# Optimization experiments

Measured on AMD Instinct MI355X. Metric: run time of the kernel, lower is better.

Reference implementation:

```python
import jax, jax.numpy as jnp
import numpy as np

S_LEN = 1024; HIDDEN = 2048; VOCAB = 32000; DFF = 6144
NK = 8; NV = 16; DK = 128; DV = 128; CONV_K = 4
CONV_DIM = 2 * NK * DK + NV * DV  # 4096
NQ = 16; NKV = 2; HD = 128; MAX_KV = 4096; SP = 512; CHUNK = 64


def silu(x):
    return x * jax.nn.sigmoid(x)


def rmsnorm(x, w, eps=1e-6):
    xf = x.astype(jnp.float32)
    return (xf * jax.lax.rsqrt(jnp.mean(xf * xf, -1, keepdims=True) + eps)) * w


def gated_rmsnorm(x, z, w, eps=1e-6):
    xf = x.astype(jnp.float32) * silu(z.astype(jnp.float32))
    return (xf * jax.lax.rsqrt(jnp.mean(xf * xf, -1, keepdims=True) + eps)) * w


def rotate_half(x):
    a, b = jnp.split(x, 2, -1)
    return jnp.concatenate([-b, a], -1)


def chunk_gated_delta_rule(q, k, v, g, beta, init_state, chunk=CHUNK):
    # q,k: [B,S,H,Dk]; v: [B,S,H,Dv]; g,beta: [B,S,H]; init_state: [B,H,Dk,Dv]
    q = q / jnp.sqrt(jnp.sum(q * q, -1, keepdims=True) + 1e-6)  # qk l2norm
    k = k / jnp.sqrt(jnp.sum(k * k, -1, keepdims=True) + 1e-6)
    tr = lambda x: x.transpose(0, 2, 1, 3).astype(jnp.float32)
    q, k, v = tr(q), tr(k), tr(v)
    g = g.transpose(0, 2, 1).astype(jnp.float32)
    beta = beta.transpose(0, 2, 1).astype(jnp.float32)
    B, H, S, Dk = q.shape
    Dv = v.shape[-1]
    N = S // chunk  # S is a multiple of chunk here (no padding needed)
    q = q * Dk ** -0.5
    rc = lambda x: x.reshape(B, H, N, chunk, x.shape[-1])
    q, k, v = rc(q), rc(k), rc(v)
    g = jnp.cumsum(g.reshape(B, H, N, chunk), -1)  # cumulative log-decay within chunk
    beta = beta.reshape(B, H, N, chunk)
    kb = k * beta[..., None]
    vb = v * beta[..., None]
    ii = jnp.arange(chunk)
    lower = ii[:, None] >= ii[None, :]
    strict = ii[:, None] > ii[None, :]
    decay = jnp.where(lower, jnp.exp(g[..., :, None] - g[..., None, :]), 0.0)
    # strictly-lower A; T = (I - A)^{-1} (exact triangular solve == converged Neumann series)
    A = -jnp.where(strict, jnp.einsum('bhnik,bhnjk->bhnij', kb, k) * decay, 0.0)
    eye = jnp.eye(chunk, dtype=jnp.float32)
    T = jax.scipy.linalg.solve_triangular(eye - A, jnp.broadcast_to(eye, A.shape), lower=True)
    w = jnp.einsum('bhnij,bhnjd->bhnid', T, vb)
    kc = jnp.einsum('bhnij,bhnjd->bhnid', T, kb * jnp.exp(g)[..., None])
    mv = lambda x: jnp.moveaxis(x, 2, 0)

    def step(state, xs):
        qi, ki, wi, kci, gi, di = xs
        attn = jnp.where(lower, jnp.einsum('bhik,bhjk->bhij', qi, ki) * di, 0.0)
        v_new = wi - jnp.einsum('bhik,bhkd->bhid', kci, state)
        out = jnp.einsum('bhik,bhkd->bhid', qi * jnp.exp(gi)[..., None], state) \
            + jnp.einsum('bhij,bhjd->bhid', attn, v_new)
        gl = gi[..., -1]
        kd = ki * jnp.exp(gl[..., None] - gi)[..., None]
        state = state * jnp.exp(gl)[..., None, None] + jnp.einsum('bhik,bhid->bhkd', kd, v_new)
        return state, out

    final, outs = jax.lax.scan(step, init_state.astype(jnp.float32),
                               (mv(q), mv(k), mv(w), mv(kc), mv(g), mv(decay)))
    out = jnp.moveaxis(outs, 0, 2).reshape(B, H, S, Dv).transpose(0, 2, 1, 3)  # [B,S,H,Dv]
    return out, final


def mlp(x, gw, uw, dw):
    return (silu(x @ gw) * (x @ uw)) @ dw


def model_forward(input_ids, start_pos, rope_cos, rope_sin, attn_mask, conv_state, rec_state,
                  key_cache, value_cache, embed_w, dl_ln_w, dl_qkv_w, conv_w, conv_b, dl_z_w,
                  dl_b_w, dl_a_w, A_log, dt_bias, dn_norm_w, dl_out_w, dl_post_ln_w, dl_gate_w,
                  dl_up_w, dl_down_w, al_ln_w, q_w, q_norm_w, k_w, k_norm_w, v_w, o_w,
                  al_post_ln_w, al_gate_w, al_up_w, al_down_w, final_norm_w, lm_head_w):
    B, S = input_ids.shape
    hidden = embed_w[input_ids]
    # ---------------- DeltaNet (linear attention) layer ----------------
    res = hidden
    x = rmsnorm(hidden, dl_ln_w)
    mixed = (x @ dl_qkv_w).transpose(0, 2, 1)             # [B, CONV_DIM, S]
    padded = jnp.concatenate([conv_state, mixed], -1)      # [B, CONV_DIM, K+S]
    L = padded.shape[-1] - (CONV_K - 1)
    conv = conv_b[:, None] + sum(conv_w[:, kk][:, None] * padded[:, :, kk:kk + L]
                                 for kk in range(CONV_K))  # depthwise conv1d
    mixed = silu(conv[:, :, -S:]).transpose(0, 2, 1)
    new_conv = padded[:, :, -CONV_K:]
    kd = NK * DK
    qq = mixed[..., :kd].reshape(B, S, NK, DK)
    kk_ = mixed[..., kd:2 * kd].reshape(B, S, NK, DK)
    vv = mixed[..., 2 * kd:].reshape(B, S, NV, DV)
    z = (x @ dl_z_w).reshape(B, S, NV, DV)
    beta = jax.nn.sigmoid(x @ dl_b_w)
    a = (x @ dl_a_w).astype(jnp.float32)
    g = -jnp.exp(A_log.astype(jnp.float32)) * jax.nn.softplus(a + dt_bias)
    rep = NV // NK
    qq = jnp.repeat(qq, rep, axis=2)
    kk_ = jnp.repeat(kk_, rep, axis=2)
    core, new_rec = chunk_gated_delta_rule(qq, kk_, vv, g, beta, rec_state)
    core = gated_rmsnorm(core.reshape(-1, DV), z.reshape(-1, DV), dn_norm_w).reshape(B, S, NV * DV)
    hidden = res + core @ dl_out_w
    hidden = hidden + mlp(rmsnorm(hidden, dl_post_ln_w), dl_gate_w, dl_up_w, dl_down_w)
    # ---------------- Full attention layer (gated GQA, KV-cache scatter) ----------------
    res = hidden
    x = rmsnorm(hidden, al_ln_w)
    qg = (x @ q_w).reshape(B, S, NQ, 2 * HD)
    query, gate = jnp.split(qg, 2, -1)
    gate = gate.reshape(B, S, NQ * HD)
    query = rmsnorm(query, q_norm_w).transpose(0, 2, 1, 3)               # [B,NQ,S,HD]
    key_new = rmsnorm((x @ k_w).reshape(B, S, NKV, HD), k_norm_w).transpose(0, 2, 1, 3)
    value_new = (x @ v_w).reshape(B, S, NKV, HD).transpose(0, 2, 1, 3)
    c = rope_cos[:, None]
    sn = rope_sin[:, None]
    query = query * c + rotate_half(query) * sn
    key_new = key_new * c + rotate_half(key_new) * sn
    new_kc = jax.lax.dynamic_update_slice(key_cache, key_new, (0, 0, start_pos, 0))
    new_vc = jax.lax.dynamic_update_slice(value_cache, value_new, (0, 0, start_pos, 0))
    ng = NQ // NKV
    k_rep = jnp.repeat(new_kc, ng, axis=1)
    v_rep = jnp.repeat(new_vc, ng, axis=1)
    scores = jnp.einsum('bhsd,bhtd->bhst', query, k_rep) * HD ** -0.5 + attn_mask
    probs = jax.nn.softmax(scores.astype(jnp.float32), -1).astype(query.dtype)
    ao = jnp.einsum('bhst,bhtd->bhsd', probs, v_rep).transpose(0, 2, 1, 3).reshape(B, S, NQ * HD)
    ao = ao * jax.nn.sigmoid(gate)
    hidden = res + ao @ o_w
    hidden = hidden + mlp(rmsnorm(hidden, al_post_ln_w), al_gate_w, al_up_w, al_down_w)
    logits = rmsnorm(hidden, final_norm_w) @ lm_head_w
    return logits, new_conv, new_rec, new_kc, new_vc


def setup_inputs():
    key = jax.random.key(0)
    ks = iter(jax.random.split(key, 64))
    def rn(shape, s=0.02):
        return jax.random.normal(next(ks), shape, jnp.float32) * s
    input_ids = jax.random.randint(next(ks), (1, S_LEN), 0, VOCAB)
    inv = 1.0 / (10000.0 ** (jnp.arange(0, HD, 2, dtype=jnp.float32) / HD))
    pos = jnp.arange(SP, SP + S_LEN, dtype=jnp.float32)
    fr = pos[:, None] * inv[None, :]
    emb = jnp.concatenate([fr, fr], -1)
    rope_cos = jnp.cos(emb)[None]
    rope_sin = jnp.sin(emb)[None]
    qpos = SP + jnp.arange(S_LEN)
    kpos = jnp.arange(MAX_KV)
    attn_mask = jnp.where(kpos[None, :] <= qpos[:, None], 0.0, -1e9).astype(jnp.float32)[None, None]
    return dict(
        input_ids=input_ids, seq_len=S_LEN, start_pos=SP,
        rope_cos=rope_cos, rope_sin=rope_sin, attn_mask=attn_mask,
        conv_state=rn((1, CONV_DIM, CONV_K), 1.0), rec_state=rn((1, NV, DK, DV), 1.0),
        key_cache=rn((1, NKV, MAX_KV, HD), 1.0), value_cache=rn((1, NKV, MAX_KV, HD), 1.0),
        embed_w=rn((VOCAB, HIDDEN)), dl_ln_w=jnp.ones(HIDDEN),
        dl_qkv_w=rn((HIDDEN, CONV_DIM)), conv_w=rn((CONV_DIM, CONV_K), 0.3),
        conv_b=rn((CONV_DIM,)), dl_z_w=rn((HIDDEN, NV * DV)),
        dl_b_w=rn((HIDDEN, NV)), dl_a_w=rn((HIDDEN, NV)),
        A_log=jnp.log(jnp.linspace(1.0, 8.0, NV)), dt_bias=rn((NV,), 0.1),
        dn_norm_w=jnp.ones(DV), dl_out_w=rn((NV * DV, HIDDEN)),
        dl_post_ln_w=jnp.ones(HIDDEN), dl_gate_w=rn((HIDDEN, DFF)),
        dl_up_w=rn((HIDDEN, DFF)), dl_down_w=rn((DFF, HIDDEN)),
        al_ln_w=jnp.ones(HIDDEN), q_w=rn((HIDDEN, NQ * HD * 2)), q_norm_w=jnp.ones(HD),
        k_w=rn((HIDDEN, NKV * HD)), k_norm_w=jnp.ones(HD), v_w=rn((HIDDEN, NKV * HD)),
        o_w=rn((NQ * HD, HIDDEN)), al_post_ln_w=jnp.ones(HIDDEN),
        al_gate_w=rn((HIDDEN, DFF)), al_up_w=rn((HIDDEN, DFF)), al_down_w=rn((DFF, HIDDEN)),
        final_norm_w=jnp.ones(HIDDEN), lm_head_w=rn((HIDDEN, VOCAB)))


def reference(input_ids, seq_len, start_pos, rope_cos, rope_sin, attn_mask, conv_state,
              rec_state, key_cache, value_cache, embed_w, dl_ln_w, dl_qkv_w, conv_w, conv_b,
              dl_z_w, dl_b_w, dl_a_w, A_log, dt_bias, dn_norm_w, dl_out_w, dl_post_ln_w,
              dl_gate_w, dl_up_w, dl_down_w, al_ln_w, q_w, q_norm_w, k_w, k_norm_w, v_w, o_w,
              al_post_ln_w, al_gate_w, al_up_w, al_down_w, final_norm_w, lm_head_w):
    del seq_len  # unused in original forward body (padding bookkeeping only)
    return model_forward(input_ids, start_pos, rope_cos, rope_sin, attn_mask, conv_state,
                         rec_state, key_cache, value_cache, embed_w, dl_ln_w, dl_qkv_w, conv_w,
                         conv_b, dl_z_w, dl_b_w, dl_a_w, A_log, dt_bias, dn_norm_w, dl_out_w,
                         dl_post_ln_w, dl_gate_w, dl_up_w, dl_down_w, al_ln_w, q_w, q_norm_w,
                         k_w, k_norm_w, v_w, o_w, al_post_ln_w, al_gate_w, al_up_w, al_down_w,
                         final_norm_w, lm_head_w)
```

## Files before the change

### kernel.cpp

```cpp
#include <hip/hip_runtime.h>
#include <math.h>

#define S_LEN 1024
#define HIDN  2048
#define NVH   16
#define CDIM  4096
#define MAXKV 4096
#define SP    512

typedef __attribute__((ext_vector_type(4))) float f32x4v;
typedef _Float16 f16x8 __attribute__((ext_vector_type(8)));
typedef unsigned short ushort_t;

__device__ __forceinline__ unsigned int pack2h(float a, float b) {
  auto h = __builtin_amdgcn_cvt_pkrtz(a, b);
  return __builtin_bit_cast(unsigned int, h);
}
__device__ __forceinline__ ushort_t h16(float x) {
  auto v = __builtin_amdgcn_cvt_pkrtz(x, x);
  return (ushort_t)__builtin_bit_cast(unsigned int, v);
}

template<bool ACC>
__global__ __launch_bounds__(256) void gemm_f16(const float* __restrict__ A,
    const float* __restrict__ B, float* __restrict__ C, int M, int N, int K) {
  __shared__ unsigned int Al[4][128][4];
  __shared__ unsigned int Bl[4][128][4];
  const int tid = threadIdx.x;
  const int gm = M >> 7;
  const int nwg = gridDim.x;
  const int q = nwg >> 3, r = nwg & 7;
  const int xcd = blockIdx.x & 7, ii = blockIdx.x >> 3;
  const int lin = (xcd < r) ? (xcd * (q + 1) + ii)
                            : (r * (q + 1) + (xcd - r) * q + ii);
  const int m0 = (lin % gm) * 128;
  const int n0 = (lin / gm) * 128;
  const int wave = tid >> 6, lane = tid & 63;
  const int wm = (wave >> 1) * 64, wn = (wave & 1) * 64;
  const int lr = lane & 15, lg = lane >> 4;
  const int am = tid >> 1, akb = (tid & 1) * 2;
  const int bn = tid & 127, bkb = (tid >> 7) * 2;
  const float* Ap = A + (size_t)(m0 + am) * K + akb * 8;
  const float* Bp = B + (size_t)(bkb * 8) * N + n0 + bn;
  float ar[16];
  float br[16];
  f32x4v acc[4][4];
  #pragma unroll
  for (int i = 0; i < 4; ++i)
    #pragma unroll
    for (int j = 0; j < 4; ++j)
      #pragma unroll
      for (int r2 = 0; r2 < 4; ++r2) acc[i][j][r2] = 0.f;
  const int NT = K >> 5;
  #pragma unroll
  for (int q2 = 0; q2 < 4; ++q2) *(float4*)&ar[q2 * 4] = *(const float4*)(Ap + q2 * 4);
  #pragma unroll
  for (int j = 0; j < 16; ++j) br[j] = Bp[(size_t)j * N];
  for (int t = 0; t < NT; ++t) {
    __syncthreads();
    *(uint4*)&Al[akb][am][0] = make_uint4(
        pack2h(ar[0], ar[1]), pack2h(ar[2], ar[3]),
        pack2h(ar[4], ar[5]), pack2h(ar[6], ar[7]));
    *(uint4*)&Al[akb + 1][am][0] = make_uint4(
        pack2h(ar[8], ar[9]), pack2h(ar[10], ar[11]),
        pack2h(ar[12], ar[13]), pack2h(ar[14], ar[15]));
    *(uint4*)&Bl[bkb][bn][0] = make_uint4(
        pack2h(br[0], br[1]), pack2h(br[2], br[3]),
        pack2h(br[4], br[5]), pack2h(br[6], br[7]));
    *(uint4*)&Bl[bkb + 1][bn][0] = make_uint4(
        pack2h(br[8], br[9]), pack2h(br[10], br[11]),
        pack2h(br[12], br[13]), pack2h(br[14], br[15]));
    if (t + 1 < NT) {
      Ap += 32; Bp += (size_t)32 * N;
      #pragma unroll
      for (int q2 = 0; q2 < 4; ++q2) *(float4*)&ar[q2 * 4] = *(const float4*)(Ap + q2 * 4);
      #pragma unroll
      for (int j = 0; j < 16; ++j) br[j] = Bp[(size_t)j * N];
    }
    __syncthreads();
    f16x8 af[4], bfr[4];
    #pragma unroll
    for (int mi = 0; mi < 4; ++mi)
      af[mi] = *(const f16x8*)&Al[lg][wm + mi * 16 + lr][0];
    #pragma unroll
    for (int ni = 0; ni < 4; ++ni)
      bfr[ni] = *(const f16x8*)&Bl[lg][wn + ni * 16 + lr][0];
    #pragma unroll
    for (int mi = 0; mi < 4; ++mi)
      #pragma unroll
      for (int ni = 0; ni < 4; ++ni)
        acc[mi][ni] = __builtin_amdgcn_mfma_f32_16x16x32_f16(
            af[mi], bfr[ni], acc[mi][ni], 0, 0, 0);
  }
  #pragma unroll
  for (int mi = 0; mi < 4; ++mi) {
    #pragma unroll
    for (int ni = 0; ni < 4; ++ni) {
      const int rr = m0 + wm + mi * 16 + lg * 4;
      const int cc = n0 + wn + ni * 16 + lr;
      #pragma unroll
      for (int r2 = 0; r2 < 4; ++r2) {
        float* cp = C + (size_t)(rr + r2) * N + cc;
        if (ACC) *cp += acc[mi][ni][r2];
        else     *cp = acc[mi][ni][r2];
      }
    }
  }
}

__global__ __launch_bounds__(256) void embed_k(const int* __restrict__ ids,
    const float* __restrict__ emb, float* __restrict__ hid) {
  int t = blockIdx.x * 256 + threadIdx.x;
  int s = t >> 9;
  int c4 = (t & 511) * 4;
  *(float4*)(hid + (size_t)s * HIDN + c4) =
      *(const float4*)(emb + (size_t)ids[s] * HIDN + c4);
}

__global__ __launch_bounds__(256) void rmsnorm_k(const float* __restrict__ in,
    const float* __restrict__ w, float* __restrict__ out) {
  const int row = blockIdx.x;
  const float* ip = in + (size_t)row * HIDN;
  float ss = 0.f;
  for (int c = threadIdx.x * 4; c < HIDN; c += 1024) {
    float4 v = *(const float4*)(ip + c);
    ss += v.x * v.x + v.y * v.y + v.z * v.z + v.w * v.w;
  }
  #pragma unroll
  for (int o = 32; o > 0; o >>= 1) ss += __shfl_down(ss, o, 64);
  __shared__ float sred[4];
  if ((threadIdx.x & 63) == 0) sred[threadIdx.x >> 6] = ss;
  __syncthreads();
  float tot = sred[0] + sred[1] + sred[2] + sred[3];
  float sc = 1.f / sqrtf(tot * (1.f / HIDN) + 1e-6f);
  for (int c = threadIdx.x * 4; c < HIDN; c += 1024) {
    float4 v = *(const float4*)(ip + c);
    float4 o = make_float4(v.x * sc * w[c], v.y * sc * w[c + 1],
                           v.z * sc * w[c + 2], v.w * sc * w[c + 3]);
    *(float4*)(out + (size_t)row * HIDN + c) = o;
  }
}

__global__ __launch_bounds__(256) void newconv_k(const float* __restrict__ mixed,
                                                 float* __restrict__ nc) {
  int t = blockIdx.x * 256 + threadIdx.x;
  int c = t >> 2, kk = t & 3;
  nc[t] = mixed[(size_t)(1020 + kk) * CDIM + c];
}

__global__ __launch_bounds__(256) void conv_k(const float* __restrict__ mixed,
    const float* __restrict__ cstate, const float* __restrict__ cw,
    const float* __restrict__ cb, float* __restrict__ convo) {
  int idx = blockIdx.x * 256 + threadIdx.x;
  int c = idx & (CDIM - 1);
  int s = idx >> 12;
  float acc = cb[c];
  #pragma unroll
  for (int kk = 0; kk < 4; ++kk) {
    int j = s + 1 + kk;
    float pv = (j < 4) ? cstate[c * 4 + j] : mixed[(size_t)(j - 4) * CDIM + c];
    acc = fmaf(cw[c * 4 + kk], pv, acc);
  }
  convo[(size_t)s * CDIM + c] = acc / (1.f + expf(-acc));
}

__global__ __launch_bounds__(128) void qknorm_k(const float* __restrict__ convo,
    float* __restrict__ qn, float* __restrict__ kn) {
  const int b = blockIdx.x;
  const int h8 = b & 7, s = b >> 3;
  const int d = threadIdx.x;
  float qv = convo[(size_t)s * CDIM + h8 * 128 + d];
  float kv = convo[(size_t)s * CDIM + 1024 + h8 * 128 + d];
  __shared__ float sred[4];
  float pq = qv * qv, pk = kv * kv;
  #pragma unroll
  for (int o = 32; o > 0; o >>= 1) { pq += __shfl_down(pq, o, 64); pk += __shfl_down(pk, o, 64); }
  if ((d & 63) == 0) { sred[d >> 6] = pq; sred[2 + (d >> 6)] = pk; }
  __syncthreads();
// ... 20 lines not shown
    acca = fmaf(xv, aw[(size_t)k * 16 + h], acca);
  }
  rb[part][h] = accb; ra[part][h] = acca;
  __syncthreads();
  if (threadIdx.x < 16) {
    const int hh = threadIdx.x;
    float sb = 0.f, sa = 0.f;
    for (int p = 0; p < 16; ++p) { sb += rb[p][hh]; sa += ra[p][hh]; }
    beta[(size_t)s * 16 + hh] = 1.f / (1.f + expf(-sb));
    float aa = sa + dt_bias[hh];
    float sp = (aa > 20.f) ? aa : log1pf(expf(aa));
    g[(size_t)s * 16 + hh] = -expf(A_log[hh]) * sp;
  }
}

__global__ __launch_bounds__(256) void delta_phase1(
    const float* __restrict__ qn, const float* __restrict__ kn,
    const float* __restrict__ convo, const float* __restrict__ beta,
    const float* __restrict__ g,
    float* __restrict__ Wb, ushort_t* __restrict__ KC16,
    ushort_t* __restrict__ Q16, ushort_t* __restrict__ K16,
    ushort_t* __restrict__ ATT16, float* __restrict__ GCb) {
  __shared__ float sK[64][129];
  __shared__ float sV[64][129];
  __shared__ float sQ[64][129];
  __shared__ float sT[64][64];
  __shared__ float sgc[64], sbeta[64], seg[64], sEgl[64];
  const int blk = blockIdx.x;
  const int n = blk & 15, h = blk >> 4;
  const int hq = h >> 1;
  const int r0 = n * 64;
  const int tid = threadIdx.x;
  const size_t hn = (size_t)h * 16 + n;
  for (int t = tid; t < 2048; t += 256) {
    int i = t >> 5, c4 = (t & 31) * 4;
    float4 kv = *(const float4*)(kn + ((size_t)hq * S_LEN + r0 + i) * 128 + c4);
    float4 qv = *(const float4*)(qn + ((size_t)hq * S_LEN + r0 + i) * 128 + c4);
    float4 vv = *(const float4*)(convo + (size_t)(r0 + i) * CDIM + 2048 + h * 128 + c4);
    sK[i][c4+0]=kv.x; sK[i][c4+1]=kv.y; sK[i][c4+2]=kv.z; sK[i][c4+3]=kv.w;
    sQ[i][c4+0]=qv.x; sQ[i][c4+1]=qv.y; sQ[i][c4+2]=qv.z; sQ[i][c4+3]=qv.w;
    sV[i][c4+0]=vv.x; sV[i][c4+1]=vv.y; sV[i][c4+2]=vv.z; sV[i][c4+3]=vv.w;
  }
  if (tid < 64) sbeta[tid] = beta[(size_t)(r0 + tid) * NVH + h];
  __syncthreads();
  if (tid == 0) {
    float acc = 0.f;
    for (int i = 0; i < 64; ++i) { acc += g[(size_t)(r0 + i) * NVH + h]; sgc[i] = acc; }
  }
  __syncthreads();
  if (tid < 64) {
    seg[tid] = expf(sgc[tid]);
    sEgl[tid] = expf(sgc[63] - sgc[tid]);
  }
  {
    const int ty = tid >> 4, tx = tid & 15;
    float a[4][4] = {};
    #pragma unroll 4
    for (int k = 0; k < 128; ++k) {
      float kr[4], kc_[4];
      #pragma unroll
      for (int di = 0; di < 4; ++di) kr[di] = sK[ty * 4 + di][k];
      #pragma unroll
      for (int dj = 0; dj < 4; ++dj) kc_[dj] = sK[tx * 4 + dj][k];
      #pragma unroll
      for (int di = 0; di < 4; ++di)
        #pragma unroll
        for (int dj = 0; dj < 4; ++dj)
          a[di][dj] = fmaf(kr[di], kc_[dj], a[di][dj]);
    }
    #pragma unroll
    for (int di = 0; di < 4; ++di) {
      int i = ty * 4 + di;
      #pragma unroll
      for (int dj = 0; dj < 4; ++dj) {
        int j = tx * 4 + dj;
        float v;
        if (i > j) v = sbeta[i] * a[di][dj] * expf(sgc[i] - sgc[j]);
        else v = (i == j) ? 1.f : 0.f;
        sT[i][j] = v;
      }
    }
  }
  __syncthreads();
  for (int i = 1; i < 64; ++i) {
    float acc = 0.f;
    const int c = tid;
    const bool act = (c < 64 && c <= i);
    if (act) {
      acc = (c == i) ? 1.f : 0.f;
      for (int j = c; j < i; ++j) acc -= sT[i][j] * sT[j][c];
    }
    __syncthreads();
    if (act) sT[i][c] = acc;
    __syncthreads();
  }
  for (int t = tid; t < 1024; t += 256) {
    int i = t >> 4, dg = (t & 15) * 8;
    float aw[8] = {}, ak[8] = {};
    for (int j = 0; j <= i; ++j) {
      float tv = sT[i][j] * sbeta[j];
      float te = tv * seg[j];
      #pragma unroll
      for (int u = 0; u < 8; ++u) {
        aw[u] = fmaf(tv, sV[j][dg + u], aw[u]);
        ak[u] = fmaf(te, sK[j][dg + u], ak[u]);
      }
    }
    float* wp = Wb + (hn * 64 + i) * 128 + dg;
    *(float4*)wp = make_float4(aw[0], aw[1], aw[2], aw[3]);
    *(float4*)(wp + 4) = make_float4(aw[4], aw[5], aw[6], aw[7]);
    uint4 kc = make_uint4(pack2h(-ak[0], -ak[1]), pack2h(-ak[2], -ak[3]),
                          pack2h(-ak[4], -ak[5]), pack2h(-ak[6], -ak[7]));
    *(uint4*)(KC16 + hn * 8192 + (dg >> 3) * 512 + i * 8) = kc;
  }
  for (int t = tid; t < 1024; t += 256) {
    int i = t >> 4, dg = (t & 15) * 8;
    float e = seg[i];
    uint4 qv = make_uint4(
        pack2h(sQ[i][dg] * e, sQ[i][dg + 1] * e),
        pack2h(sQ[i][dg + 2] * e, sQ[i][dg + 3] * e),
        pack2h(sQ[i][dg + 4] * e, sQ[i][dg + 5] * e),
        pack2h(sQ[i][dg + 6] * e, sQ[i][dg + 7] * e));
    *(uint4*)(Q16 + hn * 8192 + (dg >> 3) * 512 + i * 8) = qv;
  }
  for (int t = tid; t < 1024; t += 256) {
    int kv = t & 127, ib = t >> 7;
    int i0 = ib * 8;
    uint4 kk2 = make_uint4(
        pack2h(sK[i0 + 0][kv] * sEgl[i0 + 0], sK[i0 + 1][kv] * sEgl[i0 + 1]),
        pack2h(sK[i0 + 2][kv] * sEgl[i0 + 2], sK[i0 + 3][kv] * sEgl[i0 + 3]),
        pack2h(sK[i0 + 4][kv] * sEgl[i0 + 4], sK[i0 + 5][kv] * sEgl[i0 + 5]),
        pack2h(sK[i0 + 6][kv] * sEgl[i0 + 6], sK[i0 + 7][kv] * sEgl[i0 + 7]));
    *(uint4*)(K16 + hn * 8192 + ib * 1024 + kv * 8) = kk2;
  }
  __syncthreads();
  {
    const int ty = tid >> 4, tx = tid & 15;
    float a[4][4] = {};
    #pragma unroll 4
    for (int k = 0; k < 128; ++k) {
      float qr[4], kc_[4];
      #pragma unroll
      for (int di = 0; di < 4; ++di) qr[di] = sQ[ty * 4 + di][k];
      #pragma unroll
      for (int dj = 0; dj < 4; ++dj) kc_[dj] = sK[tx * 4 + dj][k];
      #pragma unroll
      for (int di = 0; di < 4; ++di)
        #pragma unroll
        for (int dj = 0; dj < 4; ++dj)
          a[di][dj] = fmaf(qr[di], kc_[dj], a[di][dj]);
    }
    #pragma unroll
    for (int di = 0; di < 4; ++di) {
      int i = ty * 4 + di;
      #pragma unroll
      for (int dj = 0; dj < 4; ++dj) {
        int j = tx * 4 + dj;
        float v = 0.f;
        if (i >= j) v = a[di][dj] * expf(sgc[i] - sgc[j]);
        sT[i][j] = v;
      }
    }
  }
  __syncthreads();
  for (int t = tid; t < 512; t += 256) {
    int i = t >> 3, jb = t & 7;
    const float* ap = &sT[i][jb * 8];
    uint4 av = make_uint4(pack2h(ap[0], ap[1]), pack2h(ap[2], ap[3]),
                          pack2h(ap[4], ap[5]), pack2h(ap[6], ap[7]));
    *(uint4*)(ATT16 + hn * 4096 + jb * 512 + i * 8) = av;
  }
  if (tid < 64) GCb[hn * 64 + tid] = sgc[tid];
}

__global__ __launch_bounds__(256) void delta_phase2(
    const ushort_t* __restrict__ KC16, const ushort_t* __restrict__ Q16,
    const ushort_t* __restrict__ K16, const ushort_t* __restrict__ ATT16,
    const float* __restrict__ Wb, const float* __restrict__ GCb,
// ... 92 lines not shown
        sVn[(row >> 3) * 256 + col * 8 + (row & 7)] = h16(aV[tn][r]);
      }
    __syncthreads();
    f32x4v aO[2];
    #pragma unroll
    for (int tn = 0; tn < 2; ++tn)
      #pragma unroll
      for (int r = 0; r < 4; ++r) aO[tn][r] = 0.f;
    #pragma unroll
    for (int c = 0; c < 4; ++c) {
      f16x8 a = *(const f16x8*)&sQ6[((c * 4 + lg) * 64 + w * 16 + lr) * 8];
      #pragma unroll
      for (int tn = 0; tn < 2; ++tn) {
        f16x8 b = *(const f16x8*)&sS[((c * 4 + lg) * 32 + tn * 16 + lr) * 8];
        aO[tn] = __builtin_amdgcn_mfma_f32_16x16x32_f16(a, b, aO[tn], 0, 0, 0);
      }
    }
    #pragma unroll
    for (int c = 0; c < 2; ++c) {
      f16x8 a = *(const f16x8*)&sAT[((c * 4 + lg) * 64 + w * 16 + lr) * 8];
      #pragma unroll
      for (int tn = 0; tn < 2; ++tn) {
        f16x8 b = *(const f16x8*)&sVn[((c * 4 + lg) * 32 + tn * 16 + lr) * 8];
        aO[tn] = __builtin_amdgcn_mfma_f32_16x16x32_f16(a, b, aO[tn], 0, 0, 0);
      }
    }
    #pragma unroll
    for (int tn = 0; tn < 2; ++tn)
      #pragma unroll
      for (int r = 0; r < 4; ++r) {
        int row = w * 16 + lg * 4 + r;
        core[(size_t)(n * 64 + row) * HIDN + h * 128 + d0 + tn * 16 + lr] = aO[tn][r];
      }
    #pragma unroll
    for (int tm = 0; tm < 2; ++tm)
      #pragma unroll
      for (int tn = 0; tn < 2; ++tn)
        #pragma unroll
        for (int r = 0; r < 4; ++r) aS[tm][tn][r] *= egl;
    #pragma unroll
    for (int tm = 0; tm < 2; ++tm) {
      #pragma unroll
      for (int c = 0; c < 2; ++c) {
        f16x8 a = *(const f16x8*)&sK6[((c * 4 + lg) * 128 + rowS0 + tm * 16 + lr) * 8];
        #pragma unroll
        for (int tn = 0; tn < 2; ++tn) {
          f16x8 b = *(const f16x8*)&sVn[((c * 4 + lg) * 32 + tn * 16 + lr) * 8];
          aS[tm][tn] = __builtin_amdgcn_mfma_f32_16x16x32_f16(a, b, aS[tm][tn], 0, 0, 0);
        }
      }
    }
    __syncthreads();
  }
  #pragma unroll
  for (int tm = 0; tm < 2; ++tm)
    #pragma unroll
    for (int tn = 0; tn < 2; ++tn)
      #pragma unroll
      for (int r = 0; r < 4; ++r) {
        int row = rowS0 + tm * 16 + lg * 4 + r;
        int col = tn * 16 + lr;
        new_rec[((size_t)h * 128 + row) * 128 + d0 + col] = aS[tm][tn][r];
      }
}

__global__ __launch_bounds__(128) void gatedrms_k(float* __restrict__ core,
    const float* __restrict__ z, const float* __restrict__ w) {
  const int b = blockIdx.x;
  const int h = b & 15, s = b >> 4;
  const int d = threadIdx.x;
  size_t idx = (size_t)s * HIDN + h * 128 + d;
  float cv = core[idx], zv = z[idx];
  float xf = cv * (zv / (1.f + expf(-zv)));
  __shared__ float sred[2];
  float ps = xf * xf;
  #pragma unroll
  for (int o = 32; o > 0; o >>= 1) ps += __shfl_down(ps, o, 64);
  if ((d & 63) == 0) sred[d >> 6] = ps;
  __syncthreads();
  float ss = sred[0] + sred[1];
  core[idx] = xf * (1.f / sqrtf(ss * (1.f / 128.f) + 1e-6f)) * w[d];
}

__global__ __launch_bounds__(256) void silumul_k(float* __restrict__ gbuf,
                                                 const float* __restrict__ ubuf) {
  int t = blockIdx.x * 256 + threadIdx.x;
  float4 gv = ((const float4*)gbuf)[t];
  float4 uv = ((const float4*)ubuf)[t];
  gv.x = gv.x / (1.f + expf(-gv.x)) * uv.x;
  gv.y = gv.y / (1.f + expf(-gv.y)) * uv.y;
  gv.z = gv.z / (1.f + expf(-gv.z)) * uv.z;
  gv.w = gv.w / (1.f + expf(-gv.w)) * uv.w;
  ((float4*)gbuf)[t] = gv;
}

__global__ __launch_bounds__(128) void qrope_k(const float* __restrict__ qg,
    const float* __restrict__ qnw, const float* __restrict__ cosb,
    const float* __restrict__ sinb, float* __restrict__ qhat,
    float* __restrict__ agate) {
  const int b = blockIdx.x;
  const int h = b & 15, s = b >> 4;
  const int d = threadIdx.x;
  float qv = qg[(size_t)s * 4096 + h * 256 + d];
  float gv = qg[(size_t)s * 4096 + h * 256 + 128 + d];
  __shared__ float sred[2];
  float ps = qv * qv;
  #pragma unroll
  for (int o = 32; o > 0; o >>= 1) ps += __shfl_down(ps, o, 64);
  if ((d & 63) == 0) sred[d >> 6] = ps;
  __syncthreads();
  float ss = sred[0] + sred[1];
  float qn_ = qv * (1.f / sqrtf(ss * (1.f / 128.f) + 1e-6f)) * qnw[d];
  __shared__ float tmp[128];
  tmp[d] = qn_;
  __syncthreads();
  float other = tmp[d ^ 64];
  float rh = (d < 64) ? -other : other;
  float c = cosb[(size_t)s * 128 + d];
  float sn = sinb[(size_t)s * 128 + d];
  qhat[((size_t)h * S_LEN + s) * 128 + d] = qn_ * c + rh * sn;
  agate[(size_t)s * HIDN + h * 128 + d] = gv;
}

__global__ __launch_bounds__(128) void kvrope_k(const float* __restrict__ kraw,
    const float* __restrict__ vraw, const float* __restrict__ knw,
    const float* __restrict__ cosb, const float* __restrict__ sinb,
    float* __restrict__ kcache, float* __restrict__ vcache) {
  const int b = blockIdx.x;
  const int h2 = b & 1, s = b >> 1;
  const int d = threadIdx.x;
  float kv = kraw[(size_t)s * 256 + h2 * 128 + d];
  __shared__ float sred[2];
  float ps = kv * kv;
  #pragma unroll
  for (int o = 32; o > 0; o >>= 1) ps += __shfl_down(ps, o, 64);
  if ((d & 63) == 0) sred[d >> 6] = ps;
  __syncthreads();
  float ss = sred[0] + sred[1];
  float kn_ = kv * (1.f / sqrtf(ss * (1.f / 128.f) + 1e-6f)) * knw[d];
  __shared__ float tmp[128];
  tmp[d] = kn_;
  __syncthreads();
  float other = tmp[d ^ 64];
  float rh = (d < 64) ? -other : other;
  size_t row = (size_t)h2 * MAXKV + SP + s;
  kcache[row * 128 + d] = kn_ * cosb[(size_t)s * 128 + d] + rh * sinb[(size_t)s * 128 + d];
  vcache[row * 128 + d] = vraw[(size_t)s * 256 + h2 * 128 + d];
}

__global__ __launch_bounds__(256) void attn_k(const float* __restrict__ qhat,
    const float* __restrict__ kcache, const float* __restrict__ vcache,
    const float* __restrict__ agate, float* __restrict__ ao) {
  __shared__ unsigned int Ql[16][64][4];
  __shared__ unsigned int Kl[16][64][4];
  __shared__ unsigned int Vl[8][128][4];
  __shared__ unsigned int Pl[8][64][4];
  const int h = blockIdx.x >> 4, qb = blockIdx.x & 15;
  const int hkv = h >> 3;
  const int tid = threadIdx.x;
  const int wave = tid >> 6, lane = tid & 63;
  const int lr = lane & 15, lg = lane >> 4;
  const float SCALE = 0.08838834764831845f;
  const float* Qb = qhat + ((size_t)h * S_LEN + qb * 64) * 128;
  #pragma unroll
  for (int it = 0; it < 4; ++it) {
    int tt = tid + it * 256;
    int row = tt >> 4, kb = tt & 15;
    float4 a = *(const float4*)(Qb + row * 128 + kb * 8);
    float4 b = *(const float4*)(Qb + row * 128 + kb * 8 + 4);
    *(uint4*)&Ql[kb][row][0] = make_uint4(
        pack2h(a.x * SCALE, a.y * SCALE), pack2h(a.z * SCALE, a.w * SCALE),
        pack2h(b.x * SCALE, b.y * SCALE), pack2h(b.z * SCALE, b.w * SCALE));
  }
  float m_run[4], l_run[4];
  #pragma unroll
  for (int r = 0; r < 4; ++r) { m_run[r] = -3.0e38f; l_run[r] = 0.f; }
  f32x4v accO[8];
  #pragma unroll
// ... 37 lines not shown
    for (int ni = 0; ni < 4; ++ni)
      #pragma unroll
      for (int r = 0; r < 4; ++r) accS[ni][r] = 0.f;
    #pragma unroll
    for (int c = 0; c < 4; ++c) {
      f16x8 aq = *(const f16x8*)&Ql[c * 4 + lg][wave * 16 + lr][0];
      #pragma unroll
      for (int ni = 0; ni < 4; ++ni) {
        f16x8 bk = *(const f16x8*)&Kl[c * 4 + lg][ni * 16 + lr][0];
        accS[ni] = __builtin_amdgcn_mfma_f32_16x16x32_f16(aq, bk, accS[ni], 0, 0, 0);
      }
    }
    const bool boundary = (kt == ntiles - 1);
    float alpha[4];
    #pragma unroll
    for (int r = 0; r < 4; ++r) {
      const int qrow = wave * 16 + lg * 4 + r;
      float tm = -3.0e38f;
      #pragma unroll
      for (int ni = 0; ni < 4; ++ni) {
        if (boundary && (ni * 16 + lr) > qrow) accS[ni][r] = -3.0e38f;
        tm = fmaxf(tm, accS[ni][r]);
      }
      tm = fmaxf(tm, __shfl_xor(tm, 1, 64));
      tm = fmaxf(tm, __shfl_xor(tm, 2, 64));
      tm = fmaxf(tm, __shfl_xor(tm, 4, 64));
      tm = fmaxf(tm, __shfl_xor(tm, 8, 64));
      float mnew = fmaxf(m_run[r], tm);
      alpha[r] = expf(m_run[r] - mnew);
      m_run[r] = mnew;
      float ls = 0.f;
      #pragma unroll
      for (int ni = 0; ni < 4; ++ni) {
        float p = expf(accS[ni][r] - mnew);
        accS[ni][r] = p;
        ls += p;
      }
      ls += __shfl_xor(ls, 1, 64);
      ls += __shfl_xor(ls, 2, 64);
      ls += __shfl_xor(ls, 4, 64);
      ls += __shfl_xor(ls, 8, 64);
      l_run[r] = l_run[r] * alpha[r] + ls;
    }
    {
      _Float16* pp = (_Float16*)Pl;
      #pragma unroll
      for (int ni = 0; ni < 4; ++ni) {
        int key = ni * 16 + lr;
        int base = (key >> 3) * 512 + (key & 7);
        #pragma unroll
        for (int r = 0; r < 4; ++r) {
          int q = wave * 16 + lg * 4 + r;
          pp[base + q * 8] = (_Float16)accS[ni][r];
        }
      }
    }
    #pragma unroll
    for (int nd = 0; nd < 8; ++nd)
      #pragma unroll
      for (int r = 0; r < 4; ++r) accO[nd][r] *= alpha[r];
    #pragma unroll
    for (int c2 = 0; c2 < 2; ++c2) {
      f16x8 ap = *(const f16x8*)&Pl[c2 * 4 + lg][wave * 16 + lr][0];
      #pragma unroll
      for (int nd = 0; nd < 8; ++nd) {
        f16x8 bv = *(const f16x8*)&Vl[c2 * 4 + lg][nd * 16 + lr][0];
        accO[nd] = __builtin_amdgcn_mfma_f32_16x16x32_f16(ap, bv, accO[nd], 0, 0, 0);
      }
    }
  }
  #pragma unroll
  for (int r = 0; r < 4; ++r) {
    const int s = qb * 64 + wave * 16 + lg * 4 + r;
    const float inv = 1.f / l_run[r];
    #pragma unroll
    for (int nd = 0; nd < 8; ++nd) {
      int d = nd * 16 + lr;
      float gv = agate[(size_t)s * HIDN + h * 128 + d];
      ao[(size_t)s * HIDN + h * 128 + d] = accO[nd][r] * inv * (1.f / (1.f + expf(-gv)));
    }
  }
}

static inline void gemm(const float* A, const float* B, float* C,
                        int M, int N, int K, bool acc, hipStream_t st) {
  dim3 g((N / 128) * (M / 128));
  if (acc) hipLaunchKernelGGL((gemm_f16<true>),  g, dim3(256), 0, st, A, B, C, M, N, K);
  else     hipLaunchKernelGGL((gemm_f16<false>), g, dim3(256), 0, st, A, B, C, M, N, K);
}

extern "C" void kernel_launch(void* const* d_in, const int* in_sizes, int n_in,
                              void* d_out, int out_size, void* d_ws, size_t ws_size,
                              hipStream_t stream) {
  (void)in_sizes; (void)n_in; (void)out_size; (void)ws_size;
  const int*   ids         = (const int*)  d_in[0];
  const float* rope_cos    = (const float*)d_in[3];
  const float* rope_sin    = (const float*)d_in[4];
  const float* conv_state  = (const float*)d_in[6];
  const float* rec_state   = (const float*)d_in[7];
  const float* key_cache   = (const float*)d_in[8];
  const float* value_cache = (const float*)d_in[9];
  const float* embed_w     = (const float*)d_in[10];
  const float* dl_ln_w     = (const float*)d_in[11];
  const float* dl_qkv_w    = (const float*)d_in[12];
  const float* conv_w      = (const float*)d_in[13];
  const float* conv_b      = (const float*)d_in[14];
  const float* dl_z_w      = (const float*)d_in[15];
  const float* dl_b_w      = (const float*)d_in[16];
  const float* dl_a_w      = (const float*)d_in[17];
  const float* A_log       = (const float*)d_in[18];
  const float* dt_bias     = (const float*)d_in[19];
  const float* dn_norm_w   = (const float*)d_in[20];
  const float* dl_out_w    = (const float*)d_in[21];
  const float* dl_post_ln  = (const float*)d_in[22];
  const float* dl_gate_w   = (const float*)d_in[23];
  const float* dl_up_w     = (const float*)d_in[24];
  const float* dl_down_w   = (const float*)d_in[25];
  const float* al_ln_w     = (const float*)d_in[26];
  const float* q_w         = (const float*)d_in[27];
  const float* q_norm_w    = (const float*)d_in[28];
  const float* k_w         = (const float*)d_in[29];
  const float* k_norm_w    = (const float*)d_in[30];
  const float* v_w         = (const float*)d_in[31];
  const float* o_w         = (const float*)d_in[32];
  const float* al_post_ln  = (const float*)d_in[33];
  const float* al_gate_w   = (const float*)d_in[34];
  const float* al_up_w     = (const float*)d_in[35];
  const float* al_down_w   = (const float*)d_in[36];
  const float* final_norm  = (const float*)d_in[37];
  const float* lm_head_w   = (const float*)d_in[38];

  float* out = (float*)d_out;
  float* logits   = out;
  float* new_conv = out + 32768000;
  float* new_rec  = out + 32784384;
  float* new_kc   = out + 33046528;
  float* new_vc   = out + 34095104;

  float* A_mixed = logits;
  float* A_convo = logits + 4194304;
  float* A_z     = logits + 8388608;
  float* A_qn    = logits + 10485760;
  float* A_kn    = logits + 11534336;
  float* A_w     = logits + 12582912;
  float* A_kc    = logits + 14680064;
  float* A_att   = logits + 16777216;
  float* A_gc    = logits + 17825792;
  float* A_core  = logits + 17842176;
  float* A_big0  = logits + 19939328;
  float* A_big1  = logits + 26230784;
  float* A_qhat  = A_big1;
  float* A_gate  = A_big1 + 2097152;
  float* A_ao    = A_big1 + 4194304;
  float* A_kraw  = A_mixed;
  float* A_vraw  = A_mixed + 262144;

  ushort_t* KC16  = (ushort_t*)A_kc;
  ushort_t* K16   = (ushort_t*)A_kc + 2097152;
  ushort_t* Q16   = (ushort_t*)A_att;
  ushort_t* ATT16 = (ushort_t*)A_big0;

  float* ws     = (float*)d_ws;
  float* W_hid  = ws;
  float* W_x    = ws + 2097152;
  float* W_beta = ws + 4194304;
  float* W_g    = ws + 4210688;

  hipLaunchKernelGGL(embed_k, dim3(2048), dim3(256), 0, stream, ids, embed_w, W_hid);
  hipLaunchKernelGGL(rmsnorm_k, dim3(1024), dim3(256), 0, stream, W_hid, dl_ln_w, W_x);
  gemm(W_x, dl_qkv_w, A_mixed, 1024, 4096, 2048, false, stream);
  hipLaunchKernelGGL(newconv_k, dim3(64), dim3(256), 0, stream, A_mixed, new_conv);
  hipLaunchKernelGGL(conv_k, dim3(16384), dim3(256), 0, stream,
                     A_mixed, conv_state, conv_w, conv_b, A_convo);
  gemm(W_x, dl_z_w, A_z, 1024, 2048, 2048, false, stream);
  hipLaunchKernelGGL(betag_k, dim3(1024), dim3(256), 0, stream,
                     W_x, dl_b_w, dl_a_w, A_log, dt_bias, W_beta, W_g);
  hipLaunchKernelGGL(qknorm_k, dim3(8192), dim3(128), 0, stream, A_convo, A_qn, A_kn);
  hipLaunchKernelGGL(delta_phase1, dim3(256), dim3(256), 0, stream,
                     A_qn, A_kn, A_convo, W_beta, W_g,
                     A_w, KC16, Q16, K16, ATT16, A_gc);
  hipLaunchKernelGGL(delta_phase2, dim3(64), dim3(256), 0, stream,
                     KC16, Q16, K16, ATT16, A_w, A_gc, rec_state, A_core, new_rec);
  hipLaunchKernelGGL(gatedrms_k, dim3(16384), dim3(128), 0, stream, A_core, A_z, dn_norm_w);
  gemm(A_core, dl_out_w, W_hid, 1024, 2048, 2048, true, stream);
  hipLaunchKernelGGL(rmsnorm_k, dim3(1024), dim3(256), 0, stream, W_hid, dl_post_ln, W_x);
  gemm(W_x, dl_gate_w, A_big0, 1024, 6144, 2048, false, stream);
  gemm(W_x, dl_up_w,   A_big1, 1024, 6144, 2048, false, stream);
  hipLaunchKernelGGL(silumul_k, dim3(6144), dim3(256), 0, stream, A_big0, A_big1);
  gemm(A_big0, dl_down_w, W_hid, 1024, 2048, 6144, true, stream);
  hipLaunchKernelGGL(rmsnorm_k, dim3(1024), dim3(256), 0, stream, W_hid, al_ln_w, W_x);
  gemm(W_x, q_w, A_big0, 1024, 4096, 2048, false, stream);
  hipLaunchKernelGGL(qrope_k, dim3(16384), dim3(128), 0, stream,
                     A_big0, q_norm_w, rope_cos, rope_sin, A_qhat, A_gate);
  gemm(W_x, k_w, A_kraw, 1024, 256, 2048, false, stream);
  gemm(W_x, v_w, A_vraw, 1024, 256, 2048, false, stream);
  hipMemcpyAsync(new_kc, key_cache,   (size_t)2 * MAXKV * 128 * 4, hipMemcpyDeviceToDevice, stream);
  hipMemcpyAsync(new_vc, value_cache, (size_t)2 * MAXKV * 128 * 4, hipMemcpyDeviceToDevice, stream);
  hipLaunchKernelGGL(kvrope_k, dim3(2048), dim3(128), 0, stream,
                     A_kraw, A_vraw, k_norm_w, rope_cos, rope_sin, new_kc, new_vc);
  hipLaunchKernelGGL(attn_k, dim3(256), dim3(256), 0, stream,
                     A_qhat, new_kc, new_vc, A_gate, A_ao);
  gemm(A_ao, o_w, W_hid, 1024, 2048, 2048, true, stream);
  hipLaunchKernelGGL(rmsnorm_k, dim3(1024), dim3(256), 0, stream, W_hid, al_post_ln, W_x);
  gemm(W_x, al_gate_w, A_big0, 1024, 6144, 2048, false, stream);
  gemm(W_x, al_up_w,   A_big1, 1024, 6144, 2048, false, stream);
  hipLaunchKernelGGL(silumul_k, dim3(6144), dim3(256), 0, stream, A_big0, A_big1);
  gemm(A_big0, al_down_w, W_hid, 1024, 2048, 6144, true, stream);
  hipLaunchKernelGGL(rmsnorm_k, dim3(1024), dim3(256), 0, stream, W_hid, final_norm, W_x);
  gemm(W_x, lm_head_w, logits, 1024, 32000, 2048, false, stream);
}
```

Measured before the change: 1.719 ms.

## Template GEMM on M-tile, fuse SiLU-mul into down-proj, single-wave triangular solve

The GEMM kernel gains an M-tile template parameter, so mid-sized projections can use 64-row tiles and launch more workgroups. A fused mode applies silu(gate)*up while staging the A operand, which removes the separate silumul kernel and its full read-modify-write pass over the large intermediate buffers. Separately, the triangular inverse in delta_phase1 now runs inside one 64-thread wave without per-row block barriers. The price is recomputing SiLU for each N-tile of the down projection, and loading twice as much A data per tile there.

```diff
diff --git a/kernel.cpp b/kernel.cpp
--- a/kernel.cpp
+++ b/kernel.cpp
@@ -21,49 +21,67 @@
   return (ushort_t)__builtin_bit_cast(unsigned int, v);
 }
 
-template<bool ACC>
+template<int TM, bool ACC, bool FS>
 __global__ __launch_bounds__(256) void gemm_f16(const float* __restrict__ A,
-    const float* __restrict__ B, float* __restrict__ C, int M, int N, int K) {
-  __shared__ unsigned int Al[4][128][4];
+    const float* A2, const float* __restrict__ B,
+    float* __restrict__ C, int M, int N, int K) {
+  constexpr int MI = TM / 32;
+  constexpr int AF = TM / 8;
+  __shared__ unsigned int Al[4][TM][4];
   __shared__ unsigned int Bl[4][128][4];
   const int tid = threadIdx.x;
-  const int gm = M >> 7;
+  const int gm = M / TM;
   const int nwg = gridDim.x;
   const int q = nwg >> 3, r = nwg & 7;
   const int xcd = blockIdx.x & 7, ii = blockIdx.x >> 3;
   const int lin = (xcd < r) ? (xcd * (q + 1) + ii)
                             : (r * (q + 1) + (xcd - r) * q + ii);
-  const int m0 = (lin % gm) * 128;
+  const int m0 = (lin % gm) * TM;
   const int n0 = (lin / gm) * 128;
   const int wave = tid >> 6, lane = tid & 63;
-  const int wm = (wave >> 1) * 64, wn = (wave & 1) * 64;
+  const int wm = (wave >> 1) * (TM / 2), wn = (wave & 1) * 64;
   const int lr = lane & 15, lg = lane >> 4;
-  const int am = tid >> 1, akb = (tid & 1) * 2;
+  const int am  = (TM == 128) ? (tid >> 1) : (tid >> 2);
+  const int akb = (TM == 128) ? ((tid & 1) * 2) : (tid & 3);
   const int bn = tid & 127, bkb = (tid >> 7) * 2;
-  const float* Ap = A + (size_t)(m0 + am) * K + akb * 8;
+  const float* Ap  = A + (size_t)(m0 + am) * K + akb * 8;
+  const float* A2p = A2 + (size_t)(m0 + am) * K + akb * 8;
   const float* Bp = B + (size_t)(bkb * 8) * N + n0 + bn;
-  float ar[16];
-  float br[16];
-  f32x4v acc[4][4];
-  #pragma unroll
-  for (int i = 0; i < 4; ++i)
+  float ar[AF], ar2[FS ? AF : 1], br[16];
+  f32x4v acc[MI][4];
+  #pragma unroll
+  for (int i = 0; i < MI; ++i)
     #pragma unroll
     for (int j = 0; j < 4; ++j)
       #pragma unroll
       for (int r2 = 0; r2 < 4; ++r2) acc[i][j][r2] = 0.f;
   const int NT = K >> 5;
   #pragma unroll
-  for (int q2 = 0; q2 < 4; ++q2) *(float4*)&ar[q2 * 4] = *(const float4*)(Ap + q2 * 4);
+  for (int q2 = 0; q2 < AF / 4; ++q2)
+    *(float4*)&ar[q2 * 4] = *(const float4*)(Ap + q2 * 4);
+  if (FS) {
+    #pragma unroll
+    for (int q2 = 0; q2 < AF / 4; ++q2)
+      *(float4*)&ar2[q2 * 4] = *(const float4*)(A2p + q2 * 4);
+  }
   #pragma unroll
   for (int j = 0; j < 16; ++j) br[j] = Bp[(size_t)j * N];
   for (int t = 0; t < NT; ++t) {
     __syncthreads();
+    float av[AF];
+    #pragma unroll
+    for (int u = 0; u < AF; ++u) {
+      float g = ar[u];
+      av[u] = FS ? (g / (1.f + expf(-g))) * ar2[u] : g;
+    }
     *(uint4*)&Al[akb][am][0] = make_uint4(
-        pack2h(ar[0], ar[1]), pack2h(ar[2], ar[3]),
-        pack2h(ar[4], ar[5]), pack2h(ar[6], ar[7]));
-    *(uint4*)&Al[akb + 1][am][0] = make_uint4(
-        pack2h(ar[8], ar[9]), pack2h(ar[10], ar[11]),
-        pack2h(ar[12], ar[13]), pack2h(ar[14], ar[15]));
+        pack2h(av[0], av[1]), pack2h(av[2], av[3]),
+        pack2h(av[4], av[5]), pack2h(av[6], av[7]));
+    if (TM == 128) {
+      *(uint4*)&Al[akb + 1][am][0] = make_uint4(
+          pack2h(av[8], av[9]), pack2h(av[10], av[11]),
+          pack2h(av[12], av[13]), pack2h(av[14], av[15]));
+    }
     *(uint4*)&Bl[bkb][bn][0] = make_uint4(
         pack2h(br[0], br[1]), pack2h(br[2], br[3]),
         pack2h(br[4], br[5]), pack2h(br[6], br[7]));
@@ -71,29 +89,35 @@
         pack2h(br[8], br[9]), pack2h(br[10], br[11]),
         pack2h(br[12], br[13]), pack2h(br[14], br[15]));
     if (t + 1 < NT) {
-      Ap += 32; Bp += (size_t)32 * N;
-      #pragma unroll
-      for (int q2 = 0; q2 < 4; ++q2) *(float4*)&ar[q2 * 4] = *(const float4*)(Ap + q2 * 4);
+      Ap += 32; A2p += 32; Bp += (size_t)32 * N;
+      #pragma unroll
+      for (int q2 = 0; q2 < AF / 4; ++q2)
+        *(float4*)&ar[q2 * 4] = *(const float4*)(Ap + q2 * 4);
+      if (FS) {
+        #pragma unroll
+        for (int q2 = 0; q2 < AF / 4; ++q2)
+          *(float4*)&ar2[q2 * 4] = *(const float4*)(A2p + q2 * 4);
+      }
       #pragma unroll
       for (int j = 0; j < 16; ++j) br[j] = Bp[(size_t)j * N];
     }
     __syncthreads();
-    f16x8 af[4], bfr[4];
-    #pragma unroll
-    for (int mi = 0; mi < 4; ++mi)
+    f16x8 af[MI], bfr[4];
+    #pragma unroll
+    for (int mi = 0; mi < MI; ++mi)
       af[mi] = *(const f16x8*)&Al[lg][wm + mi * 16 + lr][0];
     #pragma unroll
     for (int ni = 0; ni < 4; ++ni)
       bfr[ni] = *(const f16x8*)&Bl[lg][wn + ni * 16 + lr][0];
     #pragma unroll
-    for (int mi = 0; mi < 4; ++mi)
+    for (int mi = 0; mi < MI; ++mi)
       #pragma unroll
       for (int ni = 0; ni < 4; ++ni)
         acc[mi][ni] = __builtin_amdgcn_mfma_f32_16x16x32_f16(
             af[mi], bfr[ni], acc[mi][ni], 0, 0, 0);
   }
   #pragma unroll
-  for (int mi = 0; mi < 4; ++mi) {
+  for (int mi = 0; mi < MI; ++mi) {
     #pragma unroll
     for (int ni = 0; ni < 4; ++ni) {
       const int rr = m0 + wm + mi * 16 + lg * 4;
@@ -280,18 +304,17 @@
     }
   }
   __syncthreads();
-  for (int i = 1; i < 64; ++i) {
-    float acc = 0.f;
+  if (tid < 64) {
     const int c = tid;
-    const bool act = (c < 64 && c <= i);
-    if (act) {
-      acc = (c == i) ? 1.f : 0.f;
-      for (int j = c; j < i; ++j) acc -= sT[i][j] * sT[j][c];
-    }
-    __syncthreads();
-    if (act) sT[i][c] = acc;
-    __syncthreads();
-  }
+    for (int i = 1; i < 64; ++i) {
+      if (c <= i) {
+        float acc = (c == i) ? 1.f : 0.f;
+        for (int j = c; j < i; ++j) acc -= sT[i][j] * sT[j][c];
+        sT[i][c] = acc;
+      }
+    }
+  }
+  __syncthreads();
   for (int t = tid; t < 1024; t += 256) {
     int i = t >> 4, dg = (t & 15) * 8;
     float aw[8] = {}, ak[8] = {};
@@ -550,18 +573,6 @@
   core[idx] = xf * (1.f / sqrtf(ss * (1.f / 128.f) + 1e-6f)) * w[d];
 }
 
-__global__ __launch_bounds__(256) void silumul_k(float* __restrict__ gbuf,
-                                                 const float* __restrict__ ubuf) {
-  int t = blockIdx.x * 256 + threadIdx.x;
-  float4 gv = ((const float4*)gbuf)[t];
-  float4 uv = ((const float4*)ubuf)[t];
-  gv.x = gv.x / (1.f + expf(-gv.x)) * uv.x;
-  gv.y = gv.y / (1.f + expf(-gv.y)) * uv.y;
-  gv.z = gv.z / (1.f + expf(-gv.z)) * uv.z;
-  gv.w = gv.w / (1.f + expf(-gv.w)) * uv.w;
-  ((float4*)gbuf)[t] = gv;
-}
-
 __global__ __launch_bounds__(128) void qrope_k(const float* __restrict__ qg,
     const float* __restrict__ qnw, const float* __restrict__ cosb,
     const float* __restrict__ sinb, float* __restrict__ qhat,
@@ -765,11 +776,22 @@
   }
 }
 
-static inline void gemm(const float* A, const float* B, float* C,
-                        int M, int N, int K, bool acc, hipStream_t st) {
+static inline void gemm128(const float* A, const float* B, float* C,
+                           int M, int N, int K, bool acc, hipStream_t st) {
   dim3 g((N / 128) * (M / 128));
-  if (acc) hipLaunchKernelGGL((gemm_f16<true>),  g, dim3(256), 0, st, A, B, C, M, N, K);
-  else     hipLaunchKernelGGL((gemm_f16<false>), g, dim3(256), 0, st, A, B, C, M, N, K);
+  if (acc) hipLaunchKernelGGL((gemm_f16<128, true,  false>), g, dim3(256), 0, st, A, A, B, C, M, N, K);
+  else     hipLaunchKernelGGL((gemm_f16<128, false, false>), g, dim3(256), 0, st, A, A, B, C, M, N, K);
+}
+static inline void gemm64(const float* A, const float* B, float* C,
+                          int M, int N, int K, bool acc, hipStream_t st) {
+  dim3 g((N / 128) * (M / 64));
+  if (acc) hipLaunchKernelGGL((gemm_f16<64, true,  false>), g, dim3(256), 0, st, A, A, B, C, M, N, K);
+  else     hipLaunchKernelGGL((gemm_f16<64, false, false>), g, dim3(256), 0, st, A, A, B, C, M, N, K);
+}
+static inline void gemm_dn(const float* G, const float* U, const float* B, float* C,
+                           int M, int N, int K, hipStream_t st) {
+  dim3 g((N / 128) * (M / 64));
+  hipLaunchKernelGGL((gemm_f16<64, true, true>), g, dim3(256), 0, st, G, U, B, C, M, N, K);
 }
 
 extern "C" void kernel_launch(void* const* d_in, const int* in_sizes, int n_in,
@@ -851,11 +873,11 @@
 
   hipLaunchKernelGGL(embed_k, dim3(2048), dim3(256), 0, stream, ids, embed_w, W_hid);
   hipLaunchKernelGGL(rmsnorm_k, dim3(1024), dim3(256), 0, stream, W_hid, dl_ln_w, W_x);
-  gemm(W_x, dl_qkv_w, A_mixed, 1024, 4096, 2048, false, stream);
+  gemm128(W_x, dl_qkv_w, A_mixed, 1024, 4096, 2048, false, stream);
   hipLaunchKernelGGL(newconv_k, dim3(64), dim3(256), 0, stream, A_mixed, new_conv);
   hipLaunchKernelGGL(conv_k, dim3(16384), dim3(256), 0, stream,
                      A_mixed, conv_state, conv_w, conv_b, A_convo);
-  gemm(W_x, dl_z_w, A_z, 1024, 2048, 2048, false, stream);
+  gemm64(W_x, dl_z_w, A_z, 1024, 2048, 2048, false, stream);
   hipLaunchKernelGGL(betag_k, dim3(1024), dim3(256), 0, stream,
                      W_x, dl_b_w, dl_a_w, A_log, dt_bias, W_beta, W_g);
   hipLaunchKernelGGL(qknorm_k, dim3(8192), dim3(128), 0, stream, A_convo, A_qn, A_kn);
@@ -865,30 +887,28 @@
   hipLaunchKernelGGL(delta_phase2, dim3(64), dim3(256), 0, stream,
                      KC16, Q16, K16, ATT16, A_w, A_gc, rec_state, A_core, new_rec);
   hipLaunchKernelGGL(gatedrms_k, dim3(16384), dim3(128), 0, stream, A_core, A_z, dn_norm_w);
-  gemm(A_core, dl_out_w, W_hid, 1024, 2048, 2048, true, stream);
+  gemm64(A_core, dl_out_w, W_hid, 1024, 2048, 2048, true, stream);
   hipLaunchKernelGGL(rmsnorm_k, dim3(1024), dim3(256), 0, stream, W_hid, dl_post_ln, W_x);
-  gemm(W_x, dl_gate_w, A_big0, 1024, 6144, 2048, false, stream);
-  gemm(W_x, dl_up_w,   A_big1, 1024, 6144, 2048, false, stream);
-  hipLaunchKernelGGL(silumul_k, dim3(6144), dim3(256), 0, stream, A_big0, A_big1);
-  gemm(A_big0, dl_down_w, W_hid, 1024, 2048, 6144, true, stream);
+  gemm64(W_x, dl_gate_w, A_big0, 1024, 6144, 2048, false, stream);
+  gemm64(W_x, dl_up_w,   A_big1, 1024, 6144, 2048, false, stream);
+  gemm_dn(A_big0, A_big1, dl_down_w, W_hid, 1024, 2048, 6144, stream);
   hipLaunchKernelGGL(rmsnorm_k, dim3(1024), dim3(256), 0, stream, W_hid, al_ln_w, W_x);
-  gemm(W_x, q_w, A_big0, 1024, 4096, 2048, false, stream);
+  gemm128(W_x, q_w, A_big0, 1024, 4096, 2048, false, stream);
   hipLaunchKernelGGL(qrope_k, dim3(16384), dim3(128), 0, stream,
                      A_big0, q_norm_w, rope_cos, rope_sin, A_qhat, A_gate);
-  gemm(W_x, k_w, A_kraw, 1024, 256, 2048, false, stream);
-  gemm(W_x, v_w, A_vraw, 1024, 256, 2048, false, stream);
+  gemm64(W_x, k_w, A_kraw, 1024, 256, 2048, false, stream);
+  gemm64(W_x, v_w, A_vraw, 1024, 256, 2048, false, stream);
   hipMemcpyAsync(new_kc, key_cache,   (size_t)2 * MAXKV * 128 * 4, hipMemcpyDeviceToDevice, stream);
   hipMemcpyAsync(new_vc, value_cache, (size_t)2 * MAXKV * 128 * 4, hipMemcpyDeviceToDevice, stream);
   hipLaunchKernelGGL(kvrope_k, dim3(2048), dim3(128), 0, stream,
                      A_kraw, A_vraw, k_norm_w, rope_cos, rope_sin, new_kc, new_vc);
   hipLaunchKernelGGL(attn_k, dim3(256), dim3(256), 0, stream,
                      A_qhat, new_kc, new_vc, A_gate, A_ao);
-  gemm(A_ao, o_w, W_hid, 1024, 2048, 2048, true, stream);
+  gemm64(A_ao, o_w, W_hid, 1024, 2048, 2048, true, stream);
   hipLaunchKernelGGL(rmsnorm_k, dim3(1024), dim3(256), 0, stream, W_hid, al_post_ln, W_x);
-  gemm(W_x, al_gate_w, A_big0, 1024, 6144, 2048, false, stream);
-  gemm(W_x, al_up_w,   A_big1, 1024, 6144, 2048, false, stream);
-  hipLaunchKernelGGL(silumul_k, dim3(6144), dim3(256), 0, stream, A_big0, A_big1);
-  gemm(A_big0, al_down_w, W_hid, 1024, 2048, 6144, true, stream);
+  gemm64(W_x, al_gate_w, A_big0, 1024, 6144, 2048, false, stream);
+  gemm64(W_x, al_up_w,   A_big1, 1024, 6144, 2048, false, stream);
+  gemm_dn(A_big0, A_big1, al_down_w, W_hid, 1024, 2048, 6144, stream);
   hipLaunchKernelGGL(rmsnorm_k, dim3(1024), dim3(256), 0, stream, W_hid, final_norm, W_x);
-  gemm(W_x, lm_head_w, logits, 1024, 32000, 2048, false, stream);
-}
+  gemm128(W_x, lm_head_w, logits, 1024, 32000, 2048, false, stream);
+}
```

After: 1.733 ms. No clear change (+0.8%).
